# Performance work log

Measured on AMD Instinct MI355X. Metric: run time of the kernel, lower is better.

## Reference

```python
import jax, jax.numpy as jnp
import numpy as np

# irreps config: input = 32x0e + 16x1o ; hidden feature = 128x0e + 64x1o (+64 0e gates)
N0_IN, N1_IN = 32, 16
N0_H, N1_H = 128, 64          # scalars / vectors after each Gate
S_TP = N0_H + N1_H            # 192 scalar outputs of each hidden TensorSquare (features + gates)


def _pair_feats(s, v):
    """Symmetric tensor-square features.
    s: [N, n0] scalars, v: [N, n1, 3] l=1 vectors.
    Returns ([N, P00+P11] scalar pair features, [N, n0*n1, 3] vector pair features).
    Paths: 0e*0e->0e (u<=v products), 1o.1o->0e (u<=v dots / sqrt(3), the 3j symbol),
    0e*1o->1o (all u,w products)."""
    N, n0 = s.shape
    n1 = v.shape[1]
    iu0, iv0 = np.triu_indices(n0)
    iu1, iv1 = np.triu_indices(n1)
    ss = s[:, iu0] * s[:, iv0]                                 # [N, P00]
    dots = jnp.einsum('nui,nvi->nuv', v, v) / float(np.sqrt(3.0))
    dd = dots[:, iu1, iv1]                                     # [N, P11]
    sv = jnp.einsum('nu,nwi->nuwi', s, v).reshape(N, n0 * n1, 3)
    return jnp.concatenate([ss, dd], axis=-1), sv


def _tensor_square(s, v, W0, W1):
    """Weighted TensorSquare with 'component' normalization (1/sqrt(#paths))."""
    ps, pv = _pair_feats(s, v)
    out_s = (ps @ W0.T) / float(np.sqrt(W0.shape[1]))          # [N, m0]
    out_v = jnp.einsum('npi,mp->nmi', pv, W1) / float(np.sqrt(W1.shape[1]))  # [N, m1, 3]
    return out_s, out_v


def _gate(out_s, out_v, n_scalars):
    """e3nn Gate: silu on even scalars, sigmoid(gates) scaling the l=1 vectors."""
    scal = jax.nn.silu(out_s[:, :n_scalars])
    g = jax.nn.sigmoid(out_s[:, n_scalars:])
    return scal, g[:, :, None] * out_v


def setup_inputs() -> dict:
    key = jax.random.key(0)
    ks = jax.random.split(key, 6)
    N = 32768
    P0_1 = 528 + 136   # 664
    P1_1 = N0_IN * N1_IN  # 512
    P0_2 = 8256 + 2080  # 10336
    P1_2 = N0_H * N1_H  # 8192
    return {
        'x': jax.random.normal(ks[0], (N, N0_IN + 3 * N1_IN), dtype=jnp.float32),
        'W0_1': jax.random.normal(ks[1], (S_TP, P0_1), dtype=jnp.float32),
        'W1_1': jax.random.normal(ks[2], (N1_H, P1_1), dtype=jnp.float32),
        'W0_2': jax.random.normal(ks[3], (S_TP, P0_2), dtype=jnp.float32),
        'W1_2': jax.random.normal(ks[4], (N1_H, P1_2), dtype=jnp.float32),
        'W0_f': jax.random.normal(ks[5], (1, P0_2), dtype=jnp.float32),
    }


def reference(x, W0_1, W1_1, W0_2, W1_2, W0_f):
    N = x.shape[0]
    s = x[:, :N0_IN]
    v = x[:, N0_IN:].reshape(N, N1_IN, 3)
    # layer 1: TensorSquare -> Gate
    os, ov = _tensor_square(s, v, W0_1, W1_1)
    s, v = _gate(os, ov, N0_H)
    # layer 2 (hidden): TensorSquare -> Gate
    os, ov = _tensor_square(s, v, W0_2, W1_2)
    s, v = _gate(os, ov, N0_H)
    # final TensorSquare to irreps_out = 0e (scalar paths only)
    ps, _ = _pair_feats(s, v)
    return (ps @ W0_f.T) / float(np.sqrt(W0_f.shape[1]))       # [N, 1]
```

## Files before the change

### kernel.cpp

```cpp
#include <hip/hip_runtime.h>
#include <cstdint>
#include <cmath>

using u16 = unsigned short;
typedef __attribute__((ext_vector_type(8))) short  short8;
typedef __attribute__((ext_vector_type(4))) float  f32x4;

constexpr int NR   = 32768;
constexpr int N0I  = 32,  N1I = 16;
constexpr int N0H  = 128, N1H = 64, STP = 192;
constexpr int P00_1 = 528, P11_1 = 136, P0_1 = 664;
constexpr int P1_1  = 512;
constexpr int P00_2 = 8256, P11_2 = 2080, P0_2 = 10336;
constexpr int P1_2  = 8192;
constexpr int NCH_SS = P00_2 / 32;
constexpr int NCH    = P0_2 / 32;
constexpr int NCH1   = P1_2 / 32;
constexpr int NCH_L1 = 21;
constexpr int NCH_V1 = P1_1 / 32;

constexpr float INV_SQRT3 = 0.57735026918962576f;

constexpr size_t O_MSS2 = 0;
constexpr size_t O_MDD2 = O_MSS2 + (size_t)P00_2 * 2;
constexpr size_t O_MC1  = O_MDD2 + (size_t)P11_2 * 2;
constexpr size_t O_W01F = 22528;
constexpr size_t O_W11F = O_W01F + (size_t)NCH_L1 * 12 * 1024 * 2;
constexpr size_t O_W0F  = O_W11F + (size_t)NCH_V1 * 4 * 1024 * 2;
constexpr size_t O_W1F  = O_W0F + (size_t)NCH * 12 * 1024 * 2;
constexpr size_t O_WFM  = O_W1F + (size_t)NCH1 * 4 * 1024 * 2;
constexpr size_t O_WFD  = O_WFM + (size_t)32 * 1024 * 2;
constexpr size_t O_S1   = O_WFD + (size_t)8 * 1024 * 2;
constexpr size_t O_V1   = O_S1 + (size_t)NR * N0H * 4;
constexpr size_t O_S2   = O_V1 + (size_t)NR * (N1H * 3) * 4;
constexpr size_t O_G1   = O_S2;
constexpr size_t O_G2   = O_S2 + (size_t)NR * N0H * 4;
constexpr size_t O_V2   = O_G2 + (size_t)NR * N1H * 4;
constexpr size_t WS_NEED = O_V2 + (size_t)NR * (N1H * 3) * 4;

__device__ __forceinline__ unsigned short f2bf(float x) {
  unsigned u = __float_as_uint(x);
  u += 0x7fffu + ((u >> 16) & 1u);
  return (unsigned short)(u >> 16);
}
__device__ __forceinline__ float bf2f(unsigned short h) {
  return __uint_as_float(((unsigned)h) << 16);
}
__device__ __forceinline__ unsigned cvt_pk_bf16(float lo, float hi) {
  unsigned r;
  asm("v_cvt_pk_bf16_f32 %0, %1, %2" : "=v"(r) : "v"(lo), "v"(hi));
  return r;
}

__global__ void k_init_maps(u16* mss2, u16* mdd2, u16* mc1) {
  const int t = threadIdx.x;
  if (t < N0H) { int u = t, base = u*N0H - u*(u-1)/2;
    for (int v = u; v < N0H; ++v) mss2[base + v - u] = (u16)((u<<8)|v); }
  if (t < N1H) { int u = t, base = u*N1H - u*(u-1)/2;
    for (int v = u; v < N1H; ++v) mdd2[base + v - u] = (u16)((u<<8)|v); }
  if (t < N0I) { int u = t, base = u*N0I - u*(u-1)/2;
    for (int v = u; v < N0I; ++v) mc1[base + v - u] = (u16)((u<<8)|v); }
  if (t < N1I) { int u = t, base = u*N1I - u*(u-1)/2;
    for (int v = u; v < N1I; ++v) mc1[P00_1 + base + v - u] = (u16)(0x8000 | (u<<8) | v); }
  if (t < 8) mc1[P0_1 + t] = 0xFFFF;
}

__global__ __launch_bounds__(256) void k_prep_b(const float* __restrict__ w0_2, short* __restrict__ w0f) {
  const int g = blockIdx.x * 4 + (threadIdx.x >> 6);
  const int lane = threadIdx.x & 63;
  if (g >= NCH * 12) return;
  const int c = g / 12, nf = g - c * 12;
  const int k = c * 32 + (lane >> 4) * 8;
  const int n = nf * 16 + (lane & 15);
  const float* src = &w0_2[(size_t)n * P0_2 + k];
  float4 f0 = *(const float4*)src;
  float4 f1 = *(const float4*)(src + 4);
  const float v[8] = {f0.x, f0.y, f0.z, f0.w, f1.x, f1.y, f1.z, f1.w};
  short8 h, l;
  #pragma unroll
  for (int j = 0; j < 8; ++j) {
    unsigned short hh = f2bf(v[j]);
    h[j] = (short)hh;
    l[j] = (short)f2bf(v[j] - bf2f(hh));
  }
  short* dst = w0f + (size_t)g * 1024 + lane * 8;
  *(short8*)dst = h;
  *(short8*)(dst + 512) = l;
}

__global__ __launch_bounds__(256) void k_prep_b1v(const float* __restrict__ w1_2, short* __restrict__ w1f) {
  const int g = blockIdx.x * 4 + (threadIdx.x >> 6);
  const int lane = threadIdx.x & 63;
  if (g >= NCH1 * 4) return;
  const int c = g >> 2, nf = g & 3;
  const int k = c * 32 + (lane >> 4) * 8;
  const int n = nf * 16 + (lane & 15);
  const float* src = &w1_2[(size_t)n * P1_2 + k];
  float4 f0 = *(const float4*)src;
  float4 f1 = *(const float4*)(src + 4);
  const float v[8] = {f0.x, f0.y, f0.z, f0.w, f1.x, f1.y, f1.z, f1.w};
  short8 h, l;
  #pragma unroll
  for (int j = 0; j < 8; ++j) {
    unsigned short hh = f2bf(v[j]);
    h[j] = (short)hh;
    l[j] = (short)f2bf(v[j] - bf2f(hh));
  }
  short* dst = w1f + (size_t)g * 1024 + lane * 8;
  *(short8*)dst = h;
  *(short8*)(dst + 512) = l;
}

__global__ __launch_bounds__(256) void k_prep_b01(const float* __restrict__ w0_1, short* __restrict__ w01f) {
  const int g = blockIdx.x * 4 + (threadIdx.x >> 6);
  const int lane = threadIdx.x & 63;
  if (g >= NCH_L1 * 12) return;
  const int c = g / 12, nf = g - c * 12;
  const int k = c * 32 + (lane >> 4) * 8;
  const int n = nf * 16 + (lane & 15);
  short8 h, l;
  if (k + 8 <= P0_1) {
    const float* src = &w0_1[(size_t)n * P0_1 + k];
    float4 f0 = *(const float4*)src;
    float4 f1 = *(const float4*)(src + 4);
    const float v[8] = {f0.x, f0.y, f0.z, f0.w, f1.x, f1.y, f1.z, f1.w};
    #pragma unroll
    for (int j = 0; j < 8; ++j) {
      unsigned short hh = f2bf(v[j]);
      h[j] = (short)hh;
      l[j] = (short)f2bf(v[j] - bf2f(hh));
    }
  } else {
    #pragma unroll
    for (int j = 0; j < 8; ++j) { h[j] = 0; l[j] = 0; }
  }
  short* dst = w01f + (size_t)g * 1024 + lane * 8;
  *(short8*)dst = h;
  *(short8*)(dst + 512) = l;
}

__global__ __launch_bounds__(256) void k_prep_b11(const float* __restrict__ w1_1, short* __restrict__ w11f) {
  const int g = blockIdx.x * 4 + (threadIdx.x >> 6);
  const int lane = threadIdx.x & 63;
  if (g >= NCH_V1 * 4) return;
  const int c = g >> 2, nf = g & 3;
  const int k = c * 32 + (lane >> 4) * 8;
  const int n = nf * 16 + (lane & 15);
  const float* src = &w1_1[(size_t)n * P1_1 + k];
  float4 f0 = *(const float4*)src;
  float4 f1 = *(const float4*)(src + 4);
  const float v[8] = {f0.x, f0.y, f0.z, f0.w, f1.x, f1.y, f1.z, f1.w};
  short8 h, l;
  #pragma unroll
  for (int j = 0; j < 8; ++j) {
    unsigned short hh = f2bf(v[j]);
    h[j] = (short)hh;
    l[j] = (short)f2bf(v[j] - bf2f(hh));
  }
  short* dst = w11f + (size_t)g * 1024 + lane * 8;
  *(short8*)dst = h;
  *(short8*)(dst + 512) = l;
}

__global__ __launch_bounds__(256) void k_prep_wfm(const float* __restrict__ wf, short* __restrict__ wfm) {
  const int g = blockIdx.x * 4 + (threadIdx.x >> 6);
  const int lane = threadIdx.x & 63;
  if (g >= 32) return;
  const int c = g >> 3, nf = g & 7;
  const int k0 = c * 32 + (lane >> 4) * 8;
  const int n = nf * 16 + (lane & 15);
  short8 h, l;
  #pragma unroll
  for (int j = 0; j < 8; ++j) {
    const int k = k0 + j;
    const int u = k < n ? k : n, v = k < n ? n : k;
    float val = wf[u*N0H - u*(u-1)/2 + (v - u)];
    if (k != n) val *= 0.5f;
    unsigned short hh = f2bf(val);
    h[j] = (short)hh;
    l[j] = (short)f2bf(val - bf2f(hh));
  }
  short* dst = wfm + (size_t)g * 1024 + lane * 8;
  *(short8*)dst = h;
  *(short8*)(dst + 512) = l;
}
__global__ __launch_bounds__(256) void k_prep_wfd(const float* __restrict__ wf, short* __restrict__ wfd) {
  const int g = blockIdx.x * 4 + (threadIdx.x >> 6);
  const int lane = threadIdx.x & 63;
  if (g >= 8) return;
  const int c = g >> 2, nf = g & 3;
  const int k0 = c * 32 + (lane >> 4) * 8;
  const int n = nf * 16 + (lane & 15);
  short8 h, l;
  #pragma unroll
  for (int j = 0; j < 8; ++j) {
    const int k = k0 + j;
    const int u = k < n ? k : n, v = k < n ? n : k;
    float val = wf[P00_2 + u*N1H - u*(u-1)/2 + (v - u)] * INV_SQRT3;
    if (k != n) val *= 0.5f;
    unsigned short hh = f2bf(val);
    h[j] = (short)hh;
    l[j] = (short)f2bf(val - bf2f(hh));
  }
  short* dst = wfd + (size_t)g * 1024 + lane * 8;
  *(short8*)dst = h;
  *(short8*)(dst + 512) = l;
}

__global__ __launch_bounds__(256) void k_layer1s_mfma(
    const float* __restrict__ x,
    const short* __restrict__ w01f,
    const u16* __restrict__ mc1,
    float* __restrict__ s1, float* __restrict__ g1)
{
  __shared__ float sS[64*33];
  __shared__ float sV[64*49];
  __shared__ __align__(16) short sA[2][2048];

  const int tid  = threadIdx.x;
  const int lane = tid & 63, wid = tid >> 6;
  const int wm = wid & 1, wn = wid >> 1;
  const int r0 = blockIdx.x * 64;
  const int kp = tid & 15, rg = tid >> 4;

  for (int i = tid; i < 64*80; i += 256) {
    int r = i / 80, c = i - r*80;
    float val = x[(size_t)(r0 + r)*80 + c];
    if (c < N0I) sS[r*33 + c] = val;
    else         sV[r*49 + (c - N0I)] = val;
  }

  f32x4 acc[2][6];
  #pragma unroll
  for (int mi = 0; mi < 2; ++mi)
    #pragma unroll
    for (int q = 0; q < 6; ++q) acc[mi][q] = {0.f, 0.f, 0.f, 0.f};

  auto evalf = [&](unsigned mv, int m) -> float {
    if (mv == 0xFFFFu) return 0.f;
    const int u = (mv >> 8) & 0x7F, v = mv & 255;
    if (mv & 0x8000u) {
      const float* pa = &sV[m*49 + u*3];
      const float* pb = &sV[m*49 + v*3];
      return (pa[0]*pb[0] + pa[1]*pb[1] + pa[2]*pb[2]) * INV_SQRT3;
    }
    return sS[m*33 + u] * sS[m*33 + v];
  };

  auto write_feats = [&](int buf, int c) {
    const unsigned mv2 = *(const unsigned*)(mc1 + c*32 + 2*kp);
    const unsigned m0 = mv2 & 0xFFFFu, m1 = mv2 >> 16;
    char* a0 = (char*)&sA[buf][0];
    #pragma unroll
    for (int i = 0; i < 4; ++i) {
      const int m = rg*4 + i;
      float f0 = evalf(m0, m);
      float f1 = evalf(m1, m);
      const int off = m*64 + (((kp>>2) ^ ((m>>1)&3)) << 4) + ((kp&3) << 2);
      *(unsigned*)(a0 + off) = cvt_pk_bf16(f0, f1);
    }
  };

  auto mfma_step = [&](int c, int buf) {
    const short* bb = w01f + ((size_t)c * 12 + wn * 6) * 1024 + lane * 8;
    short8 bh[6], bl[6];
    #pragma unroll
    for (int q = 0; q < 6; ++q) {
      bh[q] = *(const short8*)(bb + q*1024);
      bl[q] = *(const short8*)(bb + q*1024 + 512);
    }
    #pragma unroll
    for (int mi = 0; mi < 2; ++mi) {
      const int m = (wm*2 + mi)*16 + (lane & 15);
      const int kg = lane >> 4;
      const int off = m*64 + ((kg ^ ((m>>1)&3)) << 4);
      short8 ah = *(const short8*)((const char*)&sA[buf][0] + off);
      #pragma unroll
      for (int q = 0; q < 6; ++q) {
        acc[mi][q] = __builtin_amdgcn_mfma_f32_16x16x32_bf16(ah, bh[q], acc[mi][q], 0, 0, 0);
        acc[mi][q] = __builtin_amdgcn_mfma_f32_16x16x32_bf16(ah, bl[q], acc[mi][q], 0, 0, 0);
      }
    }
  };

  __syncthreads();
  write_feats(0, 0);
  __syncthreads();
  for (int c = 0; c < NCH_L1; ++c) {
    const int buf = c & 1;
    if (c < NCH_L1 - 1) write_feats(buf ^ 1, c + 1);
    mfma_step(c, buf);
    __syncthreads();
  }

  const float nrm = 1.0f / sqrtf((float)P0_1);
  #pragma unroll
  for (int mi = 0; mi < 2; ++mi) {
    const int rowbase = r0 + (wm*2 + mi)*16 + (lane >> 4)*4;
    #pragma unroll
    for (int q = 0; q < 6; ++q) {
      const int col = (wn*6 + q)*16 + (lane & 15);
      #pragma unroll
      for (int r = 0; r < 4; ++r) {
        float val = acc[mi][q][r] * nrm;
        float sg = 1.f / (1.f + __expf(-val));
        if (col < N0H) s1[(size_t)(rowbase + r)*N0H + col] = val * sg;
        else           g1[(size_t)(rowbase + r)*N1H + (col - N0H)] = sg;
      }
    }
  }
}

__global__ __launch_bounds__(256) void k_layer1v_f(
    const float* __restrict__ x,
    const short* __restrict__ w11f,
    const float* __restrict__ g1,
    float* __restrict__ v1)
{
  __shared__ float sS[32*33];
  __shared__ float sV[32*49];
  __shared__ float sG[32*66];
  __shared__ __align__(16) short sA[2][3072];

  const int tid = threadIdx.x, lane = tid & 63, wid = tid >> 6;
  const int wm = wid & 1, wn = wid >> 1;
  const int n0 = blockIdx.x * 32;
  const int kp = tid & 15, rg = tid >> 4;

  for (int i = tid; i < 32*80; i += 256) {
    int n = i / 80, c = i - n*80;
    float val = x[(size_t)(n0 + n)*80 + c];
    if (c < N0I) sS[n*33 + c] = val;
    else         sV[n*49 + (c - N0I)] = val;
  }
  for (int i = tid; i < 32*64; i += 256) {
    int n = i >> 6, c = i & 63;
    sG[n*66 + c] = g1[(size_t)(n0 + n)*64 + c];
  }

  f32x4 acc[3][2];
  #pragma unroll
  for (int mi = 0; mi < 3; ++mi)
    #pragma unroll
    for (int q = 0; q < 2; ++q) acc[mi][q] = {0.f, 0.f, 0.f, 0.f};

  auto gen = [&](int buf, int c) {
    const int u = c*2 + (kp >> 3);
    const int w0 = (2*kp) & 15;
    char* a0 = (char*)&sA[buf][0];
    #pragma unroll
    for (int rr = 0; rr < 6; ++rr) {
      const int row = rg*6 + rr;
      const int n = rg*2 + rr/3, i3 = rr % 3;
      const float sval = sS[n*33 + u];
      const float f0 = sval * sV[n*49 + w0*3 + i3];
      const float f1 = sval * sV[n*49 + (w0+1)*3 + i3];
      const int off = row*64 + (((kp>>2) ^ ((row>>1)&3)) << 4) + ((kp&3) << 2);
      *(unsigned*)(a0 + off) = cvt_pk_bf16(f0, f1);
    }
  };

  auto mfma_step = [&](int c, int buf) {
    const short* bb = w11f + ((size_t)c * 4 + wn * 2) * 1024 + lane * 8;
    short8 bh[2], bl[2];
    #pragma unroll
    for (int q = 0; q < 2; ++q) {
      bh[q] = *(const short8*)(bb + q*1024);
      bl[q] = *(const short8*)(bb + q*1024 + 512);
    }
    const int c15 = lane & 15, kg = lane >> 4;
    #pragma unroll
    for (int mi = 0; mi < 3; ++mi) {
      const int row = (wm*3 + mi)*16 + c15;
      const int off = row*64 + ((kg ^ ((row>>1)&3)) << 4);
      short8 ah = *(const short8*)((const char*)&sA[buf][0] + off);
      #pragma unroll
      for (int q = 0; q < 2; ++q) {
        acc[mi][q] = __builtin_amdgcn_mfma_f32_16x16x32_bf16(ah, bh[q], acc[mi][q], 0, 0, 0);
        acc[mi][q] = __builtin_amdgcn_mfma_f32_16x16x32_bf16(ah, bl[q], acc[mi][q], 0, 0, 0);
      }
    }
  };

  __syncthreads();
  gen(0, 0);
  __syncthreads();
  for (int c = 0; c < NCH_V1; ++c) {
    const int buf = c & 1;
    if (c < NCH_V1 - 1) gen(buf ^ 1, c + 1);
    mfma_step(c, buf);
    __syncthreads();
  }

  const float nrm = 1.0f / sqrtf((float)P1_1);
  const int c15 = lane & 15, lg = lane >> 4;
  #pragma unroll
  for (int mi = 0; mi < 3; ++mi) {
    #pragma unroll
    for (int q = 0; q < 2; ++q) {
      const int m = (wn*2 + q)*16 + c15;
      #pragma unroll
      for (int r = 0; r < 4; ++r) {
        const int row = (wm*3 + mi)*16 + lg*4 + r;
        const int n = row / 3, i3 = row - n*3;
        const float g = sG[n*66 + m] * nrm;
        v1[(size_t)(n0 + n)*192 + m*3 + i3] = acc[mi][q][r] * g;
      }
    }
  }
}

struct B3 { short8 b0, b1, b2; };

__global__ __launch_bounds__(256, 5) void k_l2_scalar_mfma(
    const float* __restrict__ s1, const float* __restrict__ v1,
    const short* __restrict__ w0f,
    const u16* __restrict__ mss, const u16* __restrict__ mdd,
    float* __restrict__ s2, float* __restrict__ g2)
{
  __shared__ float sSV[32*193];
  __shared__ __align__(16) short sA[2][1024];

  const int tid  = threadIdx.x;
  const int lane = tid & 63, wid = tid >> 6;
  const int wn = wid;
  const int r0 = blockIdx.x * 32;

  const int kp = tid & 15;
  const int rg = tid >> 4;

  for (int i = tid; i < 32*128; i += 256) {
    int r = i >> 7, c = i & 127;
    sSV[r*129 + c] = s1[(size_t)(r0 + r)*N0H + c];
  }

  f32x4 acc[2][3];
  #pragma unroll
  for (int mi = 0; mi < 2; ++mi)
    #pragma unroll
    for (int q = 0; q < 3; ++q) acc[mi][q] = {0.f, 0.f, 0.f, 0.f};

  auto loadB = [&](int c) -> B3 {
    const short* bb = w0f + ((size_t)c * 12 + wn * 3) * 1024 + lane * 8;
    B3 b;
    b.b0 = *(const short8*)(bb);
    b.b1 = *(const short8*)(bb + 1024);
    b.b2 = *(const short8*)(bb + 2048);
    return b;
  };

  auto write_feats_ss = [&](int buf, int c) {
    const unsigned mv = *(const unsigned*)(mss + c*32 + 2*kp);
    const int u0 = (mv >> 8) & 255,  v0 = mv & 255;
    const int u1 = (mv >> 24) & 255, v1i = (mv >> 16) & 255;
    char* a0 = (char*)&sA[buf][0];
    #pragma unroll
    for (int i = 0; i < 2; ++i) {
      const int m = rg*2 + i;
      const float* sr = &sSV[m*129];
      float f0 = sr[u0] * sr[v0];
      float f1 = sr[u1] * sr[v1i];
      const int off = m*64 + (((kp>>2) ^ ((m>>1)&3)) << 4) + ((kp&3) << 2);
      *(unsigned*)(a0 + off) = cvt_pk_bf16(f0, f1);
    }
  };
  auto write_feats_dd = [&](int buf, int c) {
    const unsigned mv = *(const unsigned*)(mdd + (c - NCH_SS)*32 + 2*kp);
    const int u0 = (mv >> 8) & 255,  v0 = mv & 255;
    const int u1 = (mv >> 24) & 255, v1i = (mv >> 16) & 255;
    char* a0 = (char*)&sA[buf][0];
    #pragma unroll
    for (int i = 0; i < 2; ++i) {
      const int m = rg*2 + i;
      const float* vr = &sSV[m*193];
      const float* pa0 = vr + u0*3; const float* pb0 = vr + v0*3;
      const float* pa1 = vr + u1*3; const float* pb1 = vr + v1i*3;
      float f0 = (pa0[0]*pb0[0] + pa0[1]*pb0[1] + pa0[2]*pb0[2]) * INV_SQRT3;
      float f1 = (pa1[0]*pb1[0] + pa1[1]*pb1[1] + pa1[2]*pb1[2]) * INV_SQRT3;
      const int off = m*64 + (((kp>>2) ^ ((m>>1)&3)) << 4) + ((kp&3) << 2);
      *(unsigned*)(a0 + off) = cvt_pk_bf16(f0, f1);
    }
  };

  auto mfma_step = [&](const B3& B, int buf) {
    #pragma unroll
    for (int mi = 0; mi < 2; ++mi) {
      const int m = mi*16 + (lane & 15);
      const int kg = lane >> 4;
      const int off = m*64 + ((kg ^ ((m>>1)&3)) << 4);
      short8 ah = *(const short8*)((const char*)&sA[buf][0] + off);
      acc[mi][0] = __builtin_amdgcn_mfma_f32_16x16x32_bf16(ah, B.b0, acc[mi][0], 0, 0, 0);
      acc[mi][1] = __builtin_amdgcn_mfma_f32_16x16x32_bf16(ah, B.b1, acc[mi][1], 0, 0, 0);
      acc[mi][2] = __builtin_amdgcn_mfma_f32_16x16x32_bf16(ah, B.b2, acc[mi][2], 0, 0, 0);
    }
  };

  __syncthreads();

  B3 Ba = loadB(0), Bb;
  write_feats_ss(0, 0);
  __syncthreads();
  for (int c = 0; c < NCH_SS; c += 2) {
    Bb = loadB(c + 1);
    write_feats_ss(1, c + 1);
    mfma_step(Ba, 0);
    __syncthreads();
    if (c + 2 < NCH_SS) { Ba = loadB(c + 2); write_feats_ss(0, c + 2); }
    mfma_step(Bb, 1);
    __syncthreads();
  }

  for (int i = tid; i < 32*192; i += 256) {
    int r = i / 192, c = i - r*192;
    sSV[r*193 + c] = v1[(size_t)(r0 + r)*192 + c];
  }
  __syncthreads();

  Ba = loadB(NCH_SS);
  write_feats_dd(0, NCH_SS);
  __syncthreads();
  for (int c = NCH_SS; c < NCH; c += 2) {
    const bool has1 = (c + 1 < NCH);
    if (has1) { Bb = loadB(c + 1); write_feats_dd(1, c + 1); }
    mfma_step(Ba, 0);
    __syncthreads();
    if (has1) {
      if (c + 2 < NCH) { Ba = loadB(c + 2); write_feats_dd(0, c + 2); }
      mfma_step(Bb, 1);
      __syncthreads();
    }
  }

  const float nrm = 1.0f / sqrtf((float)P0_2);
  #pragma unroll
  for (int mi = 0; mi < 2; ++mi) {
    const int rowbase = r0 + mi*16 + (lane >> 4)*4;
    #pragma unroll
    for (int q = 0; q < 3; ++q) {
      const int col = (wn*3 + q)*16 + (lane & 15);
      #pragma unroll
      for (int r = 0; r < 4; ++r) {
        float val = acc[mi][q][r] * nrm;
        float sg = 1.f / (1.f + __expf(-val));
        if (col < N0H) s2[(size_t)(rowbase + r)*N0H + col] = val * sg;
        else           g2[(size_t)(rowbase + r)*N1H + (col - N0H)] = sg;
      }
    }
  }
}

__global__ __launch_bounds__(256, 5) void k_l2_vector_f(
    const float* __restrict__ s1, const float* __restrict__ v1,
    const short* __restrict__ w1f,
    const float* __restrict__ g2,
    float* __restrict__ v2)
{
  __shared__ float sS[16*129];
  __shared__ float sV[16*193];
  __shared__ float sG[16*66];
  __shared__ __align__(16) short sA[2][1536];

  const int tid = threadIdx.x, lane = tid & 63, wid = tid >> 6;
  const int wn = wid;
  const int n0 = blockIdx.x * 16;
  const int kp = tid & 15, rg = tid >> 4;

  for (int i = tid; i < 16*128; i += 256) {
    int n = i >> 7, c = i & 127;
    sS[n*129 + c] = s1[(size_t)(n0 + n)*128 + c];
  }
  for (int i = tid; i < 16*192; i += 256) {
    int n = i / 192, c = i - n*192;
    sV[n*193 + c] = v1[(size_t)(n0 + n)*192 + c];
  }
  for (int i = tid; i < 16*64; i += 256) {
    int n = i >> 6, c = i & 63;
    sG[n*66 + c] = g2[(size_t)(n0 + n)*64 + c];
  }

  f32x4 acc[3];
  #pragma unroll
  for (int mi = 0; mi < 3; ++mi) acc[mi] = {0.f, 0.f, 0.f, 0.f};

  auto loadB = [&](int c) -> short8 {
    return *(const short8*)(w1f + ((size_t)c * 4 + wn) * 1024 + lane * 8);
  };

  auto gen = [&](int buf, int c) {
    const int u = c >> 1;
    const int w0 = (c & 1) * 32 + 2*kp;
    char* a0 = (char*)&sA[buf][0];
    const float sval = sS[rg*129 + u];
    #pragma unroll
    for (int i3 = 0; i3 < 3; ++i3) {
      const int row = rg*3 + i3;
      const float f0 = sval * sV[rg*193 + w0*3 + i3];
      const float f1 = sval * sV[rg*193 + (w0+1)*3 + i3];
      const int off = row*64 + (((kp>>2) ^ ((row>>1)&3)) << 4) + ((kp&3) << 2);
      *(unsigned*)(a0 + off) = cvt_pk_bf16(f0, f1);
    }
  };

  auto mfma_step = [&](short8 bh, int buf) {
    const int c15 = lane & 15, kg = lane >> 4;
    #pragma unroll
    for (int mi = 0; mi < 3; ++mi) {
      const int row = mi*16 + c15;
      const int off = row*64 + ((kg ^ ((row>>1)&3)) << 4);
      short8 ah = *(const short8*)((const char*)&sA[buf][0] + off);
      acc[mi] = __builtin_amdgcn_mfma_f32_16x16x32_bf16(ah, bh, acc[mi], 0, 0, 0);
    }
  };

  __syncthreads();
  short8 Ba = loadB(0), Bb;
  gen(0, 0);
  __syncthreads();
  for (int c = 0; c < NCH1; c += 2) {
    Bb = loadB(c + 1);
    gen(1, c + 1);
    mfma_step(Ba, 0);
    __syncthreads();
    if (c + 2 < NCH1) { Ba = loadB(c + 2); gen(0, c + 2); }
    mfma_step(Bb, 1);
    __syncthreads();
  }

  const float nrm = 1.0f / sqrtf((float)P1_2);
  const int c15 = lane & 15, lg = lane >> 4;
  #pragma unroll
  for (int mi = 0; mi < 3; ++mi) {
    const int m = wn*16 + c15;
    #pragma unroll
    for (int r = 0; r < 4; ++r) {
      const int row = mi*16 + lg*4 + r;
      const int n = row / 3, i3 = row - n*3;
      const float g = sG[n*66 + m] * nrm;
      v2[(size_t)(n0 + n)*192 + m*3 + i3] = acc[mi][r] * g;
    }
  }
}

__global__ __launch_bounds__(256) void k_final_mfma(
    const float* __restrict__ s2, const float* __restrict__ v2,
    const short* __restrict__ wfm, const short* __restrict__ wfd,
    float* __restrict__ out)
{
  __shared__ float sS2[32*129];
  __shared__ float sV2[32*193];
  __shared__ __align__(16) short sAS[4][1024];
  __shared__ __align__(16) short sAD[2][3072];
  __shared__ float psumS[32][5];
  __shared__ float psumD[96][5];

  const int tid = threadIdx.x, lane = tid & 63, wid = tid >> 6;
  const int n0 = blockIdx.x * 32;
  const int kp = tid & 15, rg = tid >> 4;
  const int c15 = lane & 15, lg = lane >> 4;

  for (int i = tid; i < 32*128; i += 256) {
    int n = i >> 7, c = i & 127;
    sS2[n*129 + c] = s2[(size_t)(n0 + n)*128 + c];
  }
  for (int i = tid; i < 32*192; i += 256) {
    int n = i / 192, c = i - n*192;
    sV2[n*193 + c] = v2[(size_t)(n0 + n)*192 + c];
  }
  __syncthreads();

  #pragma unroll
  for (int c = 0; c < 4; ++c) {
    char* a0 = (char*)&sAS[c][0];
    #pragma unroll
    for (int i = 0; i < 2; ++i) {
      const int m = rg*2 + i;
      float f0 = sS2[m*129 + c*32 + 2*kp];
      float f1 = sS2[m*129 + c*32 + 2*kp + 1];
      const int off = m*64 + (((kp>>2) ^ ((m>>1)&3)) << 4) + ((kp&3) << 2);
      *(unsigned*)(a0 + off) = cvt_pk_bf16(f0, f1);
    }
  }
  #pragma unroll
  for (int c = 0; c < 2; ++c) {
    char* a0 = (char*)&sAD[c][0];
    #pragma unroll
    for (int rr = 0; rr < 6; ++rr) {
      const int row = rg*6 + rr;
      const int n = rg*2 + rr/3, i3 = rr % 3;
      const int w0 = c*32 + 2*kp;
      float f0 = sV2[n*193 + w0*3 + i3];
      float f1 = sV2[n*193 + (w0+1)*3 + i3];
      const int off = row*64 + (((kp>>2) ^ ((row>>1)&3)) << 4) + ((kp&3) << 2);
      *(unsigned*)(a0 + off) = cvt_pk_bf16(f0, f1);
    }
  }
  __syncthreads();

  f32x4 accS[2][2];
  #pragma unroll
  for (int mi = 0; mi < 2; ++mi)
    #pragma unroll
    for (int q = 0; q < 2; ++q) accS[mi][q] = {0.f, 0.f, 0.f, 0.f};
  #pragma unroll
  for (int c = 0; c < 4; ++c) {
    #pragma unroll
    for (int q = 0; q < 2; ++q) {
      const short* bb = wfm + ((size_t)(c*8 + wid*2 + q))*1024 + lane*8;
      short8 bh = *(const short8*)(bb);
      short8 bl = *(const short8*)(bb + 512);
      #pragma unroll
      for (int mi = 0; mi < 2; ++mi) {
        const int row = mi*16 + c15;
        const int off = row*64 + ((lg ^ ((row>>1)&3)) << 4);
        short8 ah = *(const short8*)((const char*)&sAS[c][0] + off);
        accS[mi][q] = __builtin_amdgcn_mfma_f32_16x16x32_bf16(ah, bh, accS[mi][q], 0, 0, 0);
        accS[mi][q] = __builtin_amdgcn_mfma_f32_16x16x32_bf16(ah, bl, accS[mi][q], 0, 0, 0);
      }
    }
  }

  f32x4 accD[6];
  #pragma unroll
  for (int mi = 0; mi < 6; ++mi) accD[mi] = {0.f, 0.f, 0.f, 0.f};
  #pragma unroll
  for (int c = 0; c < 2; ++c) {
    const short* bb = wfd + ((size_t)(c*4 + wid))*1024 + lane*8;
    short8 bh = *(const short8*)(bb);
    short8 bl = *(const short8*)(bb + 512);
    #pragma unroll
    for (int mi = 0; mi < 6; ++mi) {
      const int row = mi*16 + c15;
      const int off = row*64 + ((lg ^ ((row>>1)&3)) << 4);
      short8 ah = *(const short8*)((const char*)&sAD[c][0] + off);
      accD[mi] = __builtin_amdgcn_mfma_f32_16x16x32_bf16(ah, bh, accD[mi], 0, 0, 0);
      accD[mi] = __builtin_amdgcn_mfma_f32_16x16x32_bf16(ah, bl, accD[mi], 0, 0, 0);
    }
  }

  #pragma unroll
  for (int mi = 0; mi < 2; ++mi) {
    #pragma unroll
    for (int r = 0; r < 4; ++r) {
      const int row = mi*16 + lg*4 + r;
      float p = 0.f;
      #pragma unroll
      for (int q = 0; q < 2; ++q) {
        const int col = (wid*2 + q)*16 + c15;
        p += accS[mi][q][r] * sS2[row*129 + col];
      }
      #pragma unroll
      for (int off = 1; off < 16; off <<= 1) p += __shfl_xor(p, off, 16);
      if (c15 == 0) psumS[row][wid] = p;
    }
  }
  #pragma unroll
  for (int mi = 0; mi < 6; ++mi) {
    #pragma unroll
    for (int r = 0; r < 4; ++r) {
      const int row = mi*16 + lg*4 + r;
      const int n = row / 3, i3 = row - n*3;
      const int col = wid*16 + c15;
      float p = accD[mi][r] * sV2[n*193 + col*3 + i3];
      #pragma unroll
      for (int off = 1; off < 16; off <<= 1) p += __shfl_xor(p, off, 16);
      if (c15 == 0) psumD[row][wid] = p;
    }
  }
  __syncthreads();

  if (tid < 32) {
    float s = 0.f;
    #pragma unroll
    for (int w = 0; w < 4; ++w) s += psumS[tid][w];
    #pragma unroll
    for (int j = 0; j < 3; ++j)
      #pragma unroll
      for (int w = 0; w < 4; ++w) s += psumD[tid*3 + j][w];
    out[n0 + tid] = s * (1.0f / sqrtf((float)P0_2));
  }
}

extern "C" void kernel_launch(void* const* d_in, const int* in_sizes, int n_in,
                              void* d_out, int out_size, void* d_ws, size_t ws_size,
                              hipStream_t stream)
{
  const float* x    = (const float*)d_in[0];
  const float* w0_1 = (const float*)d_in[1];
  const float* w1_1 = (const float*)d_in[2];
  const float* w0_2 = (const float*)d_in[3];
  const float* w1_2 = (const float*)d_in[4];
  const float* w0_f = (const float*)d_in[5];
  float* out = (float*)d_out;
  char* ws = (char*)d_ws;

  if (ws_size < WS_NEED) return;

  u16* mss2 = (u16*)(ws + O_MSS2);
  u16* mdd2 = (u16*)(ws + O_MDD2);
  u16* mc1  = (u16*)(ws + O_MC1);
  short* w01f = (short*)(ws + O_W01F);
  short* w11f = (short*)(ws + O_W11F);
  short* w0f  = (short*)(ws + O_W0F);
  short* w1f  = (short*)(ws + O_W1F);
  short* wfm  = (short*)(ws + O_WFM);
  short* wfd  = (short*)(ws + O_WFD);
  float* s1 = (float*)(ws + O_S1);
  float* v1 = (float*)(ws + O_V1);
  float* s2 = (float*)(ws + O_S2);
  float* g1 = (float*)(ws + O_G1);
  float* g2 = (float*)(ws + O_G2);
  float* v2 = (float*)(ws + O_V2);

  hipLaunchKernelGGL(k_init_maps, dim3(1), dim3(128), 0, stream, mss2, mdd2, mc1);
  hipLaunchKernelGGL(k_prep_b01, dim3((NCH_L1*12 + 3)/4), dim3(256), 0, stream, w0_1, w01f);
  hipLaunchKernelGGL(k_prep_b11, dim3(NCH_V1), dim3(256), 0, stream, w1_1, w11f);
  hipLaunchKernelGGL(k_prep_b, dim3((NCH*12 + 3)/4), dim3(256), 0, stream, w0_2, w0f);
  hipLaunchKernelGGL(k_prep_b1v, dim3(NCH1), dim3(256), 0, stream, w1_2, w1f);
  hipLaunchKernelGGL(k_prep_wfm, dim3(8), dim3(256), 0, stream, w0_f, wfm);
  hipLaunchKernelGGL(k_prep_wfd, dim3(2), dim3(256), 0, stream, w0_f, wfd);
  hipLaunchKernelGGL(k_layer1s_mfma, dim3(NR/64), dim3(256), 0, stream,
                     x, w01f, mc1, s1, g1);
  hipLaunchKernelGGL(k_layer1v_f, dim3(NR/32), dim3(256), 0, stream,
                     x, w11f, g1, v1);
  hipLaunchKernelGGL(k_l2_scalar_mfma, dim3(NR/32), dim3(256), 0, stream,
                     s1, v1, w0f, mss2, mdd2, s2, g2);
  hipLaunchKernelGGL(k_l2_vector_f, dim3(NR/16), dim3(256), 0, stream,
                     s1, v1, w1f, g2, v2);
  hipLaunchKernelGGL(k_final_mfma, dim3(NR/32), dim3(256), 0, stream,
                     s2, v2, wfm, wfd, out);
}
```

Before: 508.5 us.

## Process two K-chunks per barrier in layer-2 MFMA loops and raise MFMA priority

The layer-2 scalar and vector MFMA kernels now produce two 32-wide K chunks of features per LDS buffer stage. This halves the number of __syncthreads per unit of work, and each stage issues twice as many MFMAs. The MFMA sections are wrapped in s_setprio to favour the matrix instructions while other waves generate features. The cost is twice the LDS for the A buffers and more live B registers, so the occupancy hint in launch_bounds drops from 5 to 4 blocks.

```diff
diff --git a/kernel.cpp b/kernel.cpp
--- a/kernel.cpp
+++ b/kernel.cpp
@@ -412,14 +412,14 @@
 
 struct B3 { short8 b0, b1, b2; };
 
-__global__ __launch_bounds__(256, 5) void k_l2_scalar_mfma(
+__global__ __launch_bounds__(256, 4) void k_l2_scalar_mfma(
     const float* __restrict__ s1, const float* __restrict__ v1,
     const short* __restrict__ w0f,
     const u16* __restrict__ mss, const u16* __restrict__ mdd,
     float* __restrict__ s2, float* __restrict__ g2)
 {
   __shared__ float sSV[32*193];
-  __shared__ __align__(16) short sA[2][1024];
+  __shared__ __align__(16) short sA[2][2048];
 
   const int tid  = threadIdx.x;
   const int lane = tid & 63, wid = tid >> 6;
@@ -449,11 +449,11 @@
     return b;
   };
 
-  auto write_feats_ss = [&](int buf, int c) {
+  auto write_feats_ss = [&](int buf, int sub, int c) {
     const unsigned mv = *(const unsigned*)(mss + c*32 + 2*kp);
     const int u0 = (mv >> 8) & 255,  v0 = mv & 255;
     const int u1 = (mv >> 24) & 255, v1i = (mv >> 16) & 255;
-    char* a0 = (char*)&sA[buf][0];
+    char* a0 = (char*)&sA[buf][0] + sub*2048;
     #pragma unroll
     for (int i = 0; i < 2; ++i) {
       const int m = rg*2 + i;
@@ -464,11 +464,11 @@
       *(unsigned*)(a0 + off) = cvt_pk_bf16(f0, f1);
     }
   };
-  auto write_feats_dd = [&](int buf, int c) {
+  auto write_feats_dd = [&](int buf, int sub, int c) {
     const unsigned mv = *(const unsigned*)(mdd + (c - NCH_SS)*32 + 2*kp);
     const int u0 = (mv >> 8) & 255,  v0 = mv & 255;
     const int u1 = (mv >> 24) & 255, v1i = (mv >> 16) & 255;
-    char* a0 = (char*)&sA[buf][0];
+    char* a0 = (char*)&sA[buf][0] + sub*2048;
     #pragma unroll
     for (int i = 0; i < 2; ++i) {
       const int m = rg*2 + i;
@@ -482,12 +482,12 @@
     }
   };
 
-  auto mfma_step = [&](const B3& B, int buf) {
+  auto mfma_step = [&](const B3& B, int buf, int sub) {
     #pragma unroll
     for (int mi = 0; mi < 2; ++mi) {
       const int m = mi*16 + (lane & 15);
       const int kg = lane >> 4;
-      const int off = m*64 + ((kg ^ ((m>>1)&3)) << 4);
+      const int off = m*64 + ((kg ^ ((m>>1)&3)) << 4) + sub*2048;
       short8 ah = *(const short8*)((const char*)&sA[buf][0] + off);
       acc[mi][0] = __builtin_amdgcn_mfma_f32_16x16x32_bf16(ah, B.b0, acc[mi][0], 0, 0, 0);
       acc[mi][1] = __builtin_amdgcn_mfma_f32_16x16x32_bf16(ah, B.b1, acc[mi][1], 0, 0, 0);
@@ -497,17 +497,25 @@
 
   __syncthreads();
 
-  B3 Ba = loadB(0), Bb;
-  write_feats_ss(0, 0);
-  __syncthreads();
-  for (int c = 0; c < NCH_SS; c += 2) {
-    Bb = loadB(c + 1);
-    write_feats_ss(1, c + 1);
-    mfma_step(Ba, 0);
+  B3 B0 = loadB(0), B1 = loadB(1);
+  write_feats_ss(0, 0, 0);
+  write_feats_ss(0, 1, 1);
+  __syncthreads();
+  for (int p = 0; p < 129; ++p) {
+    const int buf = p & 1;
+    B3 N0, N1;
+    const bool more = (p < 128);
+    if (more) {
+      N0 = loadB(2*p + 2); N1 = loadB(2*p + 3);
+      write_feats_ss(buf ^ 1, 0, 2*p + 2);
+      write_feats_ss(buf ^ 1, 1, 2*p + 3);
+    }
+    __builtin_amdgcn_s_setprio(1);
+    mfma_step(B0, buf, 0);
+    mfma_step(B1, buf, 1);
+    __builtin_amdgcn_s_setprio(0);
     __syncthreads();
-    if (c + 2 < NCH_SS) { Ba = loadB(c + 2); write_feats_ss(0, c + 2); }
-    mfma_step(Bb, 1);
-    __syncthreads();
+    if (more) { B0 = N0; B1 = N1; }
   }
 
   for (int i = tid; i < 32*192; i += 256) {
@@ -516,20 +524,32 @@
   }
   __syncthreads();
 
-  Ba = loadB(NCH_SS);
-  write_feats_dd(0, NCH_SS);
-  __syncthreads();
-  for (int c = NCH_SS; c < NCH; c += 2) {
-    const bool has1 = (c + 1 < NCH);
-    if (has1) { Bb = loadB(c + 1); write_feats_dd(1, c + 1); }
-    mfma_step(Ba, 0);
+  B0 = loadB(NCH_SS); B1 = loadB(NCH_SS + 1);
+  write_feats_dd(0, 0, NCH_SS);
+  write_feats_dd(0, 1, NCH_SS + 1);
+  __syncthreads();
+  for (int p = 0; p < 32; ++p) {
+    const int buf = p & 1;
+    B3 N0, N1;
+    if (p < 31) {
+      N0 = loadB(NCH_SS + 2*p + 2); N1 = loadB(NCH_SS + 2*p + 3);
+      write_feats_dd(buf ^ 1, 0, NCH_SS + 2*p + 2);
+      write_feats_dd(buf ^ 1, 1, NCH_SS + 2*p + 3);
+    } else {
+      N0 = loadB(NCH - 1);
+      write_feats_dd(buf ^ 1, 0, NCH - 1);
+    }
+    __builtin_amdgcn_s_setprio(1);
+    mfma_step(B0, buf, 0);
+    mfma_step(B1, buf, 1);
+    __builtin_amdgcn_s_setprio(0);
     __syncthreads();
-    if (has1) {
-      if (c + 2 < NCH) { Ba = loadB(c + 2); write_feats_dd(0, c + 2); }
-      mfma_step(Bb, 1);
-      __syncthreads();
-    }
-  }
+    B0 = N0;
+    if (p < 31) B1 = N1;
+  }
+  __builtin_amdgcn_s_setprio(1);
+  mfma_step(B0, 0, 0);
+  __builtin_amdgcn_s_setprio(0);
 
   const float nrm = 1.0f / sqrtf((float)P0_2);
   #pragma unroll
@@ -549,7 +569,7 @@
   }
 }
 
-__global__ __launch_bounds__(256, 5) void k_l2_vector_f(
+__global__ __launch_bounds__(256, 4) void k_l2_vector_f(
     const float* __restrict__ s1, const float* __restrict__ v1,
     const short* __restrict__ w1f,
     const float* __restrict__ g2,
@@ -558,7 +578,7 @@
   __shared__ float sS[16*129];
   __shared__ float sV[16*193];
   __shared__ float sG[16*66];
-  __shared__ __align__(16) short sA[2][1536];
+  __shared__ __align__(16) short sA[2][3072];
 
   const int tid = threadIdx.x, lane = tid & 63, wid = tid >> 6;
   const int wn = wid;
@@ -586,10 +606,10 @@
     return *(const short8*)(w1f + ((size_t)c * 4 + wn) * 1024 + lane * 8);
   };
 
-  auto gen = [&](int buf, int c) {
+  auto gen = [&](int buf, int sub, int c) {
     const int u = c >> 1;
     const int w0 = (c & 1) * 32 + 2*kp;
-    char* a0 = (char*)&sA[buf][0];
+    char* a0 = (char*)&sA[buf][0] + sub*3072;
     const float sval = sS[rg*129 + u];
     #pragma unroll
     for (int i3 = 0; i3 < 3; ++i3) {
@@ -601,29 +621,37 @@
     }
   };
 
-  auto mfma_step = [&](short8 bh, int buf) {
+  auto mfma_step = [&](short8 bh, int buf, int sub) {
     const int c15 = lane & 15, kg = lane >> 4;
     #pragma unroll
     for (int mi = 0; mi < 3; ++mi) {
       const int row = mi*16 + c15;
-      const int off = row*64 + ((kg ^ ((row>>1)&3)) << 4);
+      const int off = row*64 + ((kg ^ ((row>>1)&3)) << 4) + sub*3072;
       short8 ah = *(const short8*)((const char*)&sA[buf][0] + off);
       acc[mi] = __builtin_amdgcn_mfma_f32_16x16x32_bf16(ah, bh, acc[mi], 0, 0, 0);
     }
   };
 
   __syncthreads();
-  short8 Ba = loadB(0), Bb;
-  gen(0, 0);
-  __syncthreads();
-  for (int c = 0; c < NCH1; c += 2) {
-    Bb = loadB(c + 1);
-    gen(1, c + 1);
-    mfma_step(Ba, 0);
+  short8 B0 = loadB(0), B1 = loadB(1);
+  gen(0, 0, 0);
+  gen(0, 1, 1);
+  __syncthreads();
+  for (int p = 0; p < 128; ++p) {
+    const int buf = p & 1;
+    short8 N0, N1;
+    const bool more = (p < 127);
+    if (more) {
+      N0 = loadB(2*p + 2); N1 = loadB(2*p + 3);
+      gen(buf ^ 1, 0, 2*p + 2);
+      gen(buf ^ 1, 1, 2*p + 3);
+    }
+    __builtin_amdgcn_s_setprio(1);
+    mfma_step(B0, buf, 0);
+    mfma_step(B1, buf, 1);
+    __builtin_amdgcn_s_setprio(0);
     __syncthreads();
-    if (c + 2 < NCH1) { Ba = loadB(c + 2); gen(0, c + 2); }
-    mfma_step(Bb, 1);
-    __syncthreads();
+    if (more) { B0 = N0; B1 = N1; }
   }
 
   const float nrm = 1.0f / sqrtf((float)P1_2);
```

Result: no change. 517.6 us (+1.8%).

## Regroup layer-2 scalar K-chunks by fixed u with padded contiguous v

Applied to the files above, without the earlier changes.

The layer-2 scalar tensor-square K dimension is reorganised so that each 32-wide chunk shares one row index u and covers 32 consecutive v values, zero-padded past the triangle edge. Feature generation then reads one broadcast s_u plus contiguous neighbours from LDS, driven by a small per-chunk metadata table kept in shared memory, instead of per-pair index maps fetched from global memory. The weight prep builds the matching padded bf16 layout and drops the unused low-part split, which halves the stored weight size. The cost is more chunks (416 instead of 323), so more MFMA work and more B-tile loads are spent on zero padding.

```diff
diff --git a/kernel.cpp b/kernel.cpp
--- a/kernel.cpp
+++ b/kernel.cpp
@@ -13,21 +13,21 @@
 constexpr int P1_1  = 512;
 constexpr int P00_2 = 8256, P11_2 = 2080, P0_2 = 10336;
 constexpr int P1_2  = 8192;
-constexpr int NCH_SS = P00_2 / 32;
-constexpr int NCH    = P0_2 / 32;
 constexpr int NCH1   = P1_2 / 32;
 constexpr int NCH_L1 = 21;
 constexpr int NCH_V1 = P1_1 / 32;
+constexpr int NCHP_SS = 320;
+constexpr int NCHP_DD = 96;
+constexpr int NCHP    = NCHP_SS + NCHP_DD;
 
 constexpr float INV_SQRT3 = 0.57735026918962576f;
 
-constexpr size_t O_MSS2 = 0;
-constexpr size_t O_MDD2 = O_MSS2 + (size_t)P00_2 * 2;
-constexpr size_t O_MC1  = O_MDD2 + (size_t)P11_2 * 2;
-constexpr size_t O_W01F = 22528;
+constexpr size_t O_CMETA = 0;
+constexpr size_t O_MC1  = 832;
+constexpr size_t O_W01F = 2304;
 constexpr size_t O_W11F = O_W01F + (size_t)NCH_L1 * 12 * 1024 * 2;
 constexpr size_t O_W0F  = O_W11F + (size_t)NCH_V1 * 4 * 1024 * 2;
-constexpr size_t O_W1F  = O_W0F + (size_t)NCH * 12 * 1024 * 2;
+constexpr size_t O_W1F  = O_W0F + (size_t)NCHP * 12 * 512 * 2;
 constexpr size_t O_WFM  = O_W1F + (size_t)NCH1 * 4 * 1024 * 2;
 constexpr size_t O_WFD  = O_WFM + (size_t)32 * 1024 * 2;
 constexpr size_t O_S1   = O_WFD + (size_t)8 * 1024 * 2;
@@ -52,12 +52,15 @@
   return r;
 }
 
-__global__ void k_init_maps(u16* mss2, u16* mdd2, u16* mc1) {
+__global__ void k_init_maps(u16* cmeta, u16* mc1) {
   const int t = threadIdx.x;
-  if (t < N0H) { int u = t, base = u*N0H - u*(u-1)/2;
-    for (int v = u; v < N0H; ++v) mss2[base + v - u] = (u16)((u<<8)|v); }
-  if (t < N1H) { int u = t, base = u*N1H - u*(u-1)/2;
-    for (int v = u; v < N1H; ++v) mdd2[base + v - u] = (u16)((u<<8)|v); }
+  if (t == 0) {
+    int c = 0;
+    for (int u = 0; u < N0H; ++u)
+      for (int v0 = u; v0 < N0H; v0 += 32) cmeta[c++] = (u16)((u << 8) | v0);
+    for (int u = 0; u < N1H; ++u)
+      for (int v0 = u; v0 < N1H; v0 += 32) cmeta[c++] = (u16)((u << 8) | v0);
+  }
   if (t < N0I) { int u = t, base = u*N0I - u*(u-1)/2;
     for (int v = u; v < N0I; ++v) mc1[base + v - u] = (u16)((u<<8)|v); }
   if (t < N1I) { int u = t, base = u*N1I - u*(u-1)/2;
@@ -65,27 +68,30 @@
   if (t < 8) mc1[P0_1 + t] = 0xFFFF;
 }
 
-__global__ __launch_bounds__(256) void k_prep_b(const float* __restrict__ w0_2, short* __restrict__ w0f) {
+__global__ __launch_bounds__(256) void k_prep_b(const float* __restrict__ w0_2,
+                                                const u16* __restrict__ cmeta,
+                                                short* __restrict__ w0f) {
   const int g = blockIdx.x * 4 + (threadIdx.x >> 6);
   const int lane = threadIdx.x & 63;
-  if (g >= NCH * 12) return;
+  if (g >= NCHP * 12) return;
   const int c = g / 12, nf = g - c * 12;
-  const int k = c * 32 + (lane >> 4) * 8;
+  const unsigned meta = cmeta[c];
+  const int u = meta >> 8, v0 = meta & 255;
+  const int kk = (lane >> 4) * 8;
   const int n = nf * 16 + (lane & 15);
-  const float* src = &w0_2[(size_t)n * P0_2 + k];
-  float4 f0 = *(const float4*)src;
-  float4 f1 = *(const float4*)(src + 4);
-  const float v[8] = {f0.x, f0.y, f0.z, f0.w, f1.x, f1.y, f1.z, f1.w};
-  short8 h, l;
+  short8 h;
   #pragma unroll
   for (int j = 0; j < 8; ++j) {
-    unsigned short hh = f2bf(v[j]);
-    h[j] = (short)hh;
-    l[j] = (short)f2bf(v[j] - bf2f(hh));
-  }
-  short* dst = w0f + (size_t)g * 1024 + lane * 8;
-  *(short8*)dst = h;
-  *(short8*)(dst + 512) = l;
+    const int v = v0 + kk + j;
+    float val = 0.f;
+    if (c < NCHP_SS) {
+      if (v < N0H) val = w0_2[(size_t)n * P0_2 + (u*N0H - u*(u-1)/2 + (v - u))];
+    } else {
+      if (v < N1H) val = w0_2[(size_t)n * P0_2 + (P00_2 + u*N1H - u*(u-1)/2 + (v - u))];
+    }
+    h[j] = (short)f2bf(val);
+  }
+  *(short8*)(w0f + (size_t)g * 512 + lane * 8) = h;
 }
 
 __global__ __launch_bounds__(256) void k_prep_b1v(const float* __restrict__ w1_2, short* __restrict__ w1f) {
@@ -415,11 +421,12 @@
 __global__ __launch_bounds__(256, 5) void k_l2_scalar_mfma(
     const float* __restrict__ s1, const float* __restrict__ v1,
     const short* __restrict__ w0f,
-    const u16* __restrict__ mss, const u16* __restrict__ mdd,
+    const u16* __restrict__ cmeta,
     float* __restrict__ s2, float* __restrict__ g2)
 {
   __shared__ float sSV[32*193];
   __shared__ __align__(16) short sA[2][1024];
+  __shared__ u16 sMeta[NCHP];
 
   const int tid  = threadIdx.x;
   const int lane = tid & 63, wid = tid >> 6;
@@ -429,9 +436,10 @@
   const int kp = tid & 15;
   const int rg = tid >> 4;
 
-  for (int i = tid; i < 32*128; i += 256) {
-    int r = i >> 7, c = i & 127;
-    sSV[r*129 + c] = s1[(size_t)(r0 + r)*N0H + c];
+  for (int i = tid; i < NCHP; i += 256) sMeta[i] = cmeta[i];
+  for (int i = tid; i < 32*161; i += 256) {
+    int r = i / 161, c = i - r*161;
+    sSV[r*161 + c] = (c < 128) ? s1[(size_t)(r0 + r)*N0H + c] : 0.f;
   }
 
   f32x4 acc[2][3];
@@ -441,42 +449,45 @@
     for (int q = 0; q < 3; ++q) acc[mi][q] = {0.f, 0.f, 0.f, 0.f};
 
   auto loadB = [&](int c) -> B3 {
-    const short* bb = w0f + ((size_t)c * 12 + wn * 3) * 1024 + lane * 8;
+    const short* bb = w0f + ((size_t)c * 12 + wn * 3) * 512 + lane * 8;
     B3 b;
     b.b0 = *(const short8*)(bb);
-    b.b1 = *(const short8*)(bb + 1024);
-    b.b2 = *(const short8*)(bb + 2048);
+    b.b1 = *(const short8*)(bb + 512);
+    b.b2 = *(const short8*)(bb + 1024);
     return b;
   };
 
-  auto write_feats_ss = [&](int buf, int c) {
-    const unsigned mv = *(const unsigned*)(mss + c*32 + 2*kp);
-    const int u0 = (mv >> 8) & 255,  v0 = mv & 255;
-    const int u1 = (mv >> 24) & 255, v1i = (mv >> 16) & 255;
+  auto gen_ss = [&](int buf, int c) {
+    const unsigned meta = sMeta[c];
+    const int u = meta >> 8;
+    const int v = (int)(meta & 255) + 2*kp;
     char* a0 = (char*)&sA[buf][0];
     #pragma unroll
     for (int i = 0; i < 2; ++i) {
       const int m = rg*2 + i;
-      const float* sr = &sSV[m*129];
-      float f0 = sr[u0] * sr[v0];
-      float f1 = sr[u1] * sr[v1i];
+      const float su = sSV[m*161 + u];
+      const float f0 = su * sSV[m*161 + v];
+      const float f1 = su * sSV[m*161 + v + 1];
       const int off = m*64 + (((kp>>2) ^ ((m>>1)&3)) << 4) + ((kp&3) << 2);
       *(unsigned*)(a0 + off) = cvt_pk_bf16(f0, f1);
     }
   };
-  auto write_feats_dd = [&](int buf, int c) {
-    const unsigned mv = *(const unsigned*)(mdd + (c - NCH_SS)*32 + 2*kp);
-    const int u0 = (mv >> 8) & 255,  v0 = mv & 255;
-    const int u1 = (mv >> 24) & 255, v1i = (mv >> 16) & 255;
+  auto gen_dd = [&](int buf, int c) {
+    const unsigned meta = sMeta[c];
+    const int u3 = (int)(meta >> 8) * 3;
+    const int v = (int)(meta & 255) + 2*kp;
+    const int va0 = (v  < 64 ? v  : 63) * 3;
+    const int va1 = (v+1 < 64 ? v+1 : 63) * 3;
     char* a0 = (char*)&sA[buf][0];
     #pragma unroll
     for (int i = 0; i < 2; ++i) {
       const int m = rg*2 + i;
       const float* vr = &sSV[m*193];
-      const float* pa0 = vr + u0*3; const float* pb0 = vr + v0*3;
-      const float* pa1 = vr + u1*3; const float* pb1 = vr + v1i*3;
-      float f0 = (pa0[0]*pb0[0] + pa0[1]*pb0[1] + pa0[2]*pb0[2]) * INV_SQRT3;
-      float f1 = (pa1[0]*pb1[0] + pa1[1]*pb1[1] + pa1[2]*pb1[2]) * INV_SQRT3;
+      const float a = vr[u3], b = vr[u3+1], cc = vr[u3+2];
+      float d0 = (a*vr[va0] + b*vr[va0+1] + cc*vr[va0+2]) * INV_SQRT3;
+      float d1 = (a*vr[va1] + b*vr[va1+1] + cc*vr[va1+2]) * INV_SQRT3;
+      const float f0 = (v   < 64) ? d0 : 0.f;
+      const float f1 = (v+1 < 64) ? d1 : 0.f;
       const int off = m*64 + (((kp>>2) ^ ((m>>1)&3)) << 4) + ((kp&3) << 2);
       *(unsigned*)(a0 + off) = cvt_pk_bf16(f0, f1);
     }
@@ -498,14 +509,14 @@
   __syncthreads();
 
   B3 Ba = loadB(0), Bb;
-  write_feats_ss(0, 0);
-  __syncthreads();
-  for (int c = 0; c < NCH_SS; c += 2) {
+  gen_ss(0, 0);
+  __syncthreads();
+  for (int c = 0; c < NCHP_SS; c += 2) {
     Bb = loadB(c + 1);
-    write_feats_ss(1, c + 1);
+    gen_ss(1, c + 1);
     mfma_step(Ba, 0);
     __syncthreads();
-    if (c + 2 < NCH_SS) { Ba = loadB(c + 2); write_feats_ss(0, c + 2); }
+    if (c + 2 < NCHP_SS) { Ba = loadB(c + 2); gen_ss(0, c + 2); }
     mfma_step(Bb, 1);
     __syncthreads();
   }
@@ -516,19 +527,17 @@
   }
   __syncthreads();
 
-  Ba = loadB(NCH_SS);
-  write_feats_dd(0, NCH_SS);
-  __syncthreads();
-  for (int c = NCH_SS; c < NCH; c += 2) {
-    const bool has1 = (c + 1 < NCH);
-    if (has1) { Bb = loadB(c + 1); write_feats_dd(1, c + 1); }
+  Ba = loadB(NCHP_SS);
+  gen_dd(0, NCHP_SS);
+  __syncthreads();
+  for (int c = NCHP_SS; c < NCHP; c += 2) {
+    Bb = loadB(c + 1);
+    gen_dd(1, c + 1);
     mfma_step(Ba, 0);
     __syncthreads();
-    if (has1) {
-      if (c + 2 < NCH) { Ba = loadB(c + 2); write_feats_dd(0, c + 2); }
-      mfma_step(Bb, 1);
-      __syncthreads();
-    }
+    if (c + 2 < NCHP) { Ba = loadB(c + 2); gen_dd(0, c + 2); }
+    mfma_step(Bb, 1);
+    __syncthreads();
   }
 
   const float nrm = 1.0f / sqrtf((float)P0_2);
@@ -795,8 +804,7 @@
 
   if (ws_size < WS_NEED) return;
 
-  u16* mss2 = (u16*)(ws + O_MSS2);
-  u16* mdd2 = (u16*)(ws + O_MDD2);
+  u16* cmeta = (u16*)(ws + O_CMETA);
   u16* mc1  = (u16*)(ws + O_MC1);
   short* w01f = (short*)(ws + O_W01F);
   short* w11f = (short*)(ws + O_W11F);
@@ -811,10 +819,10 @@
   float* g2 = (float*)(ws + O_G2);
   float* v2 = (float*)(ws + O_V2);
 
-  hipLaunchKernelGGL(k_init_maps, dim3(1), dim3(128), 0, stream, mss2, mdd2, mc1);
+  hipLaunchKernelGGL(k_init_maps, dim3(1), dim3(128), 0, stream, cmeta, mc1);
   hipLaunchKernelGGL(k_prep_b01, dim3((NCH_L1*12 + 3)/4), dim3(256), 0, stream, w0_1, w01f);
   hipLaunchKernelGGL(k_prep_b11, dim3(NCH_V1), dim3(256), 0, stream, w1_1, w11f);
-  hipLaunchKernelGGL(k_prep_b, dim3((NCH*12 + 3)/4), dim3(256), 0, stream, w0_2, w0f);
+  hipLaunchKernelGGL(k_prep_b, dim3((NCHP*12 + 3)/4), dim3(256), 0, stream, w0_2, cmeta, w0f);
   hipLaunchKernelGGL(k_prep_b1v, dim3(NCH1), dim3(256), 0, stream, w1_2, w1f);
   hipLaunchKernelGGL(k_prep_wfm, dim3(8), dim3(256), 0, stream, w0_f, wfm);
   hipLaunchKernelGGL(k_prep_wfd, dim3(2), dim3(256), 0, stream, w0_f, wfd);
@@ -823,7 +831,7 @@
   hipLaunchKernelGGL(k_layer1v_f, dim3(NR/32), dim3(256), 0, stream,
                      x, w11f, g1, v1);
   hipLaunchKernelGGL(k_l2_scalar_mfma, dim3(NR/32), dim3(256), 0, stream,
-                     s1, v1, w0f, mss2, mdd2, s2, g2);
+                     s1, v1, w0f, cmeta, s2, g2);
   hipLaunchKernelGGL(k_l2_vector_f, dim3(NR/16), dim3(256), 0, stream,
                      s1, v1, w1f, g2, v2);
   hipLaunchKernelGGL(k_final_mfma, dim3(NR/32), dim3(256), 0, stream,
```

Result: slower. 557.3 us (+9.6%).
